# Kernel optimization log

Hardware: AMD Instinct MI355X
Metric: run time of the kernel (lower is better)

The kernel has to match this reference:

```python
import jax, jax.numpy as jnp
import numpy as np

Q = 0.25          # magnetic charge q
MAX_EIGEN = 2.0   # max_eigen default

N_NODES = 1024
N_EDGES = 32768
IN_DIM = 128


def setup_inputs() -> dict:
    key = jax.random.key(0)
    k1, k2, k3, k4 = jax.random.split(key, 4)
    features = jax.random.normal(k1, (N_NODES, IN_DIM), dtype=jnp.float32)
    edges = jax.random.randint(k2, (2, N_EDGES), 0, N_NODES, dtype=jnp.int64)
    w_e1 = jax.random.normal(k3, (1, IN_DIM), dtype=jnp.float32) * (1.0 / np.sqrt(IN_DIM))
    b_e1 = jax.random.normal(k4, (1,), dtype=jnp.float32) * 0.01
    return {"features": features, "edges": edges, "w_e1": w_e1, "b_e1": b_e1, "K": 4}


def reference(features, edges, w_e1, b_e1, K):
    N = features.shape[0]
    # e1: Linear(input_dim, 1), then squeeze -> per-node scalar potential p
    p = (features @ w_e1.T + b_e1)[:, 0]                       # [N]
    u, v = edges[0], edges[1]
    val = jnp.maximum(p[u] - p[v], 0.0)                        # [M]
    w = 1.0 + val
    directed = val > 0
    # val == 0 -> self loops (u,u),(v,v); val > 0 -> (u,v),(v,u); weight 1+val each
    rows = jnp.concatenate([u, v])
    cols = jnp.concatenate([jnp.where(directed, v, u), jnp.where(directed, u, v)])
    ww = jnp.concatenate([w, w])
    A = jnp.zeros((N, N), dtype=features.dtype).at[rows, cols].add(ww)
    A = A + jnp.eye(N, dtype=features.dtype)                   # unit-weight self loops (diag_eye)

    A_sym = 0.5 * (A + A.T)
    # symmetric degree normalization (norm=True)
    d = A_sym.sum(axis=0)
    d = jnp.where(d == 0, 1.0, d) ** -0.5
    A_sym = d[:, None] * A_sym * d[None, :]

    # magnetic phase: Theta = exp(2*pi*q*i*(A - A^T))
    Theta = jnp.exp((2j * jnp.pi * Q) * (A - A.T).astype(jnp.complex64))
    I = jnp.eye(N, dtype=jnp.complex64)
    L = I - Theta * A_sym.astype(jnp.complex64)                # D=I since norm=True
    L = (2.0 / MAX_EIGEN) * L - I                              # spectral rescale

    # Chebyshev recursion: T0 = I, T1 = L, T_k = 2 L T_{k-1} - T_{k-2}
    polys = [I, L]
    for _ in range(2, K + 1):
        polys.append(2.0 * (L @ polys[-1]) - polys[-2])
    L_real = jnp.stack([t.real for t in polys])                # [K+1, N, N]
    L_img = jnp.stack([t.imag for t in polys])                 # [K+1, N, N]
    return (L_real, L_img)
```

## Files before the change

kernel.cpp:

```cpp
#include <hip/hip_runtime.h>

#define NPTS 1024
#define NN (NPTS * NPTS)
#define NEDGE 32768
#define INDIM 128
#define PAD 72

typedef __attribute__((ext_vector_type(8))) short bf16x8;
typedef __attribute__((ext_vector_type(4))) float f32x4;

__device__ inline ushort f2bf(float x) {
    union { float f; unsigned u; } v; v.f = x;
    unsigned r = (v.u + 0x7FFF + ((v.u >> 16) & 1)) >> 16;
    return (ushort)r;
}

#define MFMA(a, b, c) __builtin_amdgcn_mfma_f32_16x16x32_bf16(a, b, c, 0, 0, 0)


__global__ void zeroA_p_kernel(float4* __restrict__ A4,
                               const float* __restrict__ feat,
                               const float* __restrict__ w,
                               const float* __restrict__ b,
                               float* __restrict__ p) {
    int t = threadIdx.x;
    A4[blockIdx.x * 256 + t] = make_float4(0.f, 0.f, 0.f, 0.f);
    if (blockIdx.x < 256) {
        int wid = t >> 6, lane = t & 63;
        int node = blockIdx.x * 4 + wid;
        const float* f = feat + node * INDIM;
        float s = f[lane] * w[lane] + f[lane + 64] * w[lane + 64];
#pragma unroll
        for (int off = 32; off; off >>= 1) s += __shfl_down(s, off);
        if (lane == 0) p[node] = s + b[0];
    }
}

__global__ void build_A_kernel(const int* __restrict__ eu, const int* __restrict__ ev,
                               const float* __restrict__ p, float* __restrict__ A) {
    int i = blockIdx.x * blockDim.x + threadIdx.x;
    if (i >= NEDGE) return;
    int u = eu[i], v = ev[i];
    float val = p[u] - p[v];
    if (val > 0.f) {
        float w = 1.f + val;
        atomicAdd(&A[u * NPTS + v], w);
        atomicAdd(&A[v * NPTS + u], w);
    } else {
        atomicAdd(&A[u * NPTS + u], 1.f);
        atomicAdd(&A[v * NPTS + v], 1.f);
    }
}

__global__ void row_deg_kernel(const float* __restrict__ A, float* __restrict__ dinv) {
    int wid = threadIdx.x >> 6, lane = threadIdx.x & 63;
    int row = blockIdx.x * 4 + wid;
    const float4* r4 = (const float4*)(A + (size_t)row * NPTS);
    float s = 0.f;
#pragma unroll
    for (int c = 0; c < 4; ++c) {
        float4 v = r4[c * 64 + lane];
        s += v.x + v.y + v.z + v.w;
    }
#pragma unroll
    for (int off = 32; off; off >>= 1) s += __shfl_down(s, off);
    if (lane == 0) dinv[row] = rsqrtf(s + 1.f);
}

__global__ void normalize_kernel(const float* __restrict__ A, const float* __restrict__ dinv,
                                 float* __restrict__ out, ushort* __restrict__ Mbf) {
    int idx4 = blockIdx.x * blockDim.x + threadIdx.x;
    int i = idx4 >> 8;
    int j = (idx4 & 255) * 4;
    size_t idx = (size_t)idx4 * 4;
    float di = dinv[i];
    float4 a = *(const float4*)(A + idx);
    float4 dj = *(const float4*)(dinv + j);
    float4 t0 = make_float4(0.f, 0.f, 0.f, 0.f);
    if (i == j) t0.x = 1.f;
    else if (i == j + 1) t0.y = 1.f;
    else if (i == j + 2) t0.z = 1.f;
    else if (i == j + 3) t0.w = 1.f;
    a.x += (i == j);
    a.y += (i == j + 1);
    a.z += (i == j + 2);
    a.w += (i == j + 3);
    float4 m;
    m.x = -(di * a.x * dj.x);
    m.y = -(di * a.y * dj.y);
    m.z = -(di * a.z * dj.z);
    m.w = -(di * a.w * dj.w);
    *(float4*)(out + idx) = t0;
    *(float4*)(out + NN + idx) = m;
    ushort mb[4] = {f2bf(m.x), f2bf(m.y), f2bf(m.z), f2bf(m.w)};
    *(uint2*)(Mbf + idx) = *(uint2*)mb;
}

__global__ __launch_bounds__(512) void gemm_S_kernel(const ushort* __restrict__ Mbf,
                                                     ushort* __restrict__ Sbf,
                                                     float* __restrict__ out) {
    __shared__ __align__(16) ushort smem[4 * 64 * PAD];
    ushort(*sA)[64][PAD] = (ushort(*)[64][PAD])smem;
    ushort(*sB)[64][PAD] = (ushort(*)[64][PAD])(smem + 2 * 64 * PAD);
    float* red = (float*)smem;

    int tid = threadIdx.x;
    int brow = blockIdx.y * 64, bcol = blockIdx.x * 64;
    int r = tid >> 3, j0 = (tid & 7) * 8;
    int wid = tid >> 6, lane = tid & 63;
    int h = wid >> 2, w4 = wid & 3;
    int wr = (w4 & 1) * 32, wc = (w4 >> 1) * 32;
    int fr = lane & 15, g = lane >> 4;

    const ushort* Arow = Mbf + (size_t)(brow + r) * NPTS;
    const ushort* Brow = Mbf + (size_t)(bcol + r) * NPTS;

    f32x4 acc[2][2] = {};
    float4 pa0 = *(const float4*)(Arow + j0);
    float4 pa1 = *(const float4*)(Arow + 64 + j0);
    float4 pb0 = *(const float4*)(Brow + j0);
    float4 pb1 = *(const float4*)(Brow + 64 + j0);

    for (int it = 0; it < 8; ++it) {
        __syncthreads();
        *(float4*)&sA[0][r][j0] = pa0;
        *(float4*)&sA[1][r][j0] = pa1;
        *(float4*)&sB[0][r][j0] = pb0;
        *(float4*)&sB[1][r][j0] = pb1;
        __syncthreads();
        if (it < 7) {
            int k0 = (it + 1) * 128;
            pa0 = *(const float4*)(Arow + k0 + j0);
            pa1 = *(const float4*)(Arow + k0 + 64 + j0);
            pb0 = *(const float4*)(Brow + k0 + j0);
            pb1 = *(const float4*)(Brow + k0 + 64 + j0);
        }
#pragma unroll
        for (int kc = 0; kc < 2; ++kc) {
            int kk = kc * 32 + g * 8;
            bf16x8 a0 = *(const bf16x8*)&sA[h][wr + fr][kk];
            bf16x8 a1 = *(const bf16x8*)&sA[h][wr + 16 + fr][kk];
            bf16x8 b0 = *(const bf16x8*)&sB[h][wc + fr][kk];
            bf16x8 b1 = *(const bf16x8*)&sB[h][wc + 16 + fr][kk];
            acc[0][0] = MFMA(a0, b0, acc[0][0]);
            acc[0][1] = MFMA(a0, b1, acc[0][1]);
            acc[1][0] = MFMA(a1, b0, acc[1][0]);
            acc[1][1] = MFMA(a1, b1, acc[1][1]);
        }
    }

    __syncthreads();
    if (h == 1) {
#pragma unroll
        for (int q = 0; q < 4; ++q)
            *(f32x4*)&red[q * 1024 + (w4 * 64 + lane) * 4] = acc[q >> 1][q & 1];
    }
    __syncthreads();
    if (h == 0) {
        float* T2 = out + (size_t)2 * NN;
#pragma unroll
        for (int mi = 0; mi < 2; ++mi) {
#pragma unroll
            for (int ni = 0; ni < 2; ++ni) {
                f32x4 o = *(f32x4*)&red[(mi * 2 + ni) * 1024 + (w4 * 64 + lane) * 4];
#pragma unroll
                for (int q = 0; q < 4; ++q) {
                    int row = brow + wr + mi * 16 + g * 4 + q;
                    int col = bcol + wc + ni * 16 + fr;
                    size_t idx = (size_t)row * NPTS + col;
                    float s = acc[mi][ni][q] + o[q];
                    T2[idx] = 2.f * s - (row == col ? 1.f : 0.f);
                    Sbf[idx] = f2bf(s);
                }
            }
        }
    }
}

__global__ __launch_bounds__(512) void gemm_T34_kernel(const ushort* __restrict__ Mbf,
                                                       const ushort* __restrict__ Sbf,
                                                       float* __restrict__ out,
                                                       int zimag) {
    if (zimag) {
        int bid = blockIdx.y * 16 + blockIdx.x;
        float4* z = (float4*)(out + (size_t)5 * NN) + (size_t)bid * 5120 + threadIdx.x;
#pragma unroll
        for (int i = 0; i < 10; ++i) z[i * 512] = make_float4(0.f, 0.f, 0.f, 0.f);
    }

    __shared__ __align__(16) ushort smem[6 * 64 * PAD];
    ushort(*sAS)[64][PAD] = (ushort(*)[64][PAD])smem;
    ushort(*sAM)[64][PAD] = (ushort(*)[64][PAD])(smem + 2 * 64 * PAD);
    ushort(*sB)[64][PAD] = (ushort(*)[64][PAD])(smem + 4 * 64 * PAD);
    float* red = (float*)smem;

    int tid = threadIdx.x;
    int brow = blockIdx.y * 64, bcol = blockIdx.x * 64;
    int r = tid >> 3, j0 = (tid & 7) * 8;
    int wid = tid >> 6, lane = tid & 63;
    int h = wid >> 2, w4 = wid & 3;
    int wr = (w4 & 1) * 32, wc = (w4 >> 1) * 32;
    int fr = lane & 15, g = lane >> 4;

    const ushort* ASrow = Sbf + (size_t)(brow + r) * NPTS;
    const ushort* AMrow = Mbf + (size_t)(brow + r) * NPTS;
    const ushort* Brow = Sbf + (size_t)(bcol + r) * NPTS;

    f32x4 accP[2][2] = {};
    f32x4 accR[2][2] = {};
    float4 ps0 = *(const float4*)(ASrow + j0);
    float4 ps1 = *(const float4*)(ASrow + 64 + j0);
    float4 pm0 = *(const float4*)(AMrow + j0);
    float4 pm1 = *(const float4*)(AMrow + 64 + j0);
    float4 pb0 = *(const float4*)(Brow + j0);
    float4 pb1 = *(const float4*)(Brow + 64 + j0);

    for (int it = 0; it < 8; ++it) {
        __syncthreads();
        *(float4*)&sAS[0][r][j0] = ps0;
        *(float4*)&sAS[1][r][j0] = ps1;
        *(float4*)&sAM[0][r][j0] = pm0;
        *(float4*)&sAM[1][r][j0] = pm1;
        *(float4*)&sB[0][r][j0] = pb0;
        *(float4*)&sB[1][r][j0] = pb1;
        __syncthreads();
        if (it < 7) {
            int k0 = (it + 1) * 128;
            ps0 = *(const float4*)(ASrow + k0 + j0);
            ps1 = *(const float4*)(ASrow + k0 + 64 + j0);
            pm0 = *(const float4*)(AMrow + k0 + j0);
            pm1 = *(const float4*)(AMrow + k0 + 64 + j0);
            pb0 = *(const float4*)(Brow + k0 + j0);
            pb1 = *(const float4*)(Brow + k0 + 64 + j0);
        }
#pragma unroll
        for (int kc = 0; kc < 2; ++kc) {
            int kk = kc * 32 + g * 8;
            bf16x8 b0 = *(const bf16x8*)&sB[h][wc + fr][kk];
            bf16x8 b1 = *(const bf16x8*)&sB[h][wc + 16 + fr][kk];
            bf16x8 s0 = *(const bf16x8*)&sAS[h][wr + fr][kk];
            bf16x8 s1 = *(const bf16x8*)&sAS[h][wr + 16 + fr][kk];
            accP[0][0] = MFMA(s0, b0, accP[0][0]);
            accP[0][1] = MFMA(s0, b1, accP[0][1]);
            accP[1][0] = MFMA(s1, b0, accP[1][0]);
            accP[1][1] = MFMA(s1, b1, accP[1][1]);
            bf16x8 m0 = *(const bf16x8*)&sAM[h][wr + fr][kk];
            bf16x8 m1 = *(const bf16x8*)&sAM[h][wr + 16 + fr][kk];
            accR[0][0] = MFMA(m0, b0, accR[0][0]);
            accR[0][1] = MFMA(m0, b1, accR[0][1]);
            accR[1][0] = MFMA(m1, b0, accR[1][0]);
            accR[1][1] = MFMA(m1, b1, accR[1][1]);
        }
    }

    __syncthreads();
    if (h == 1) {
#pragma unroll
        for (int q = 0; q < 4; ++q) {
            *(f32x4*)&red[q * 1024 + (w4 * 64 + lane) * 4] = accP[q >> 1][q & 1];
            *(f32x4*)&red[4096 + q * 1024 + (w4 * 64 + lane) * 4] = accR[q >> 1][q & 1];
        }
    }
    __syncthreads();
    if (h == 0) {
        float* T1 = out + (size_t)NN;
        float* T2 = out + (size_t)2 * NN;
        float* T3 = out + (size_t)3 * NN;
        float* T4 = out + (size_t)4 * NN;
#pragma unroll
        for (int mi = 0; mi < 2; ++mi) {
#pragma unroll
            for (int ni = 0; ni < 2; ++ni) {
                f32x4 oP = *(f32x4*)&red[(mi * 2 + ni) * 1024 + (w4 * 64 + lane) * 4];
                f32x4 oR = *(f32x4*)&red[4096 + (mi * 2 + ni) * 1024 + (w4 * 64 + lane) * 4];
#pragma unroll
                for (int q = 0; q < 4; ++q) {
                    int row = brow + wr + mi * 16 + g * 4 + q;
                    int col = bcol + wc + ni * 16 + fr;
                    size_t idx = (size_t)row * NPTS + col;
                    float sp = accP[mi][ni][q] + oP[q];
                    float sr = accR[mi][ni][q] + oR[q];
                    T4[idx] = 8.f * sp - 4.f * T2[idx] - (row == col ? 3.f : 0.f);
                    T3[idx] = 4.f * sr - 3.f * T1[idx];
                }
            }
        }
    }
}

__global__ void zero_kernel(float4* __restrict__ p, int n4) {
    int i = blockIdx.x * blockDim.x + threadIdx.x;
    if (i < n4) p[i] = make_float4(0.f, 0.f, 0.f, 0.f);
}


extern "C" void kernel_launch(void* const* d_in, const int* in_sizes, int n_in,
                              void* d_out, int out_size, void* d_ws, size_t ws_size,
                              hipStream_t stream) {
    const float* feat = (const float*)d_in[0];
    const int* edges = (const int*)d_in[1];
    const float* w_e1 = (const float*)d_in[2];
    const float* b_e1 = (const float*)d_in[3];
    float* out = (float*)d_out;

    const size_t need = (size_t)NN * 4 + (size_t)NN * 2 + (size_t)NN * 2 + NPTS * 8 + 256;
    float* A;
    ushort* Mbf;
    ushort* Sbf;
    float* p;
    float* dinv;
    int use_ws = (ws_size >= need);
    if (use_ws) {
        char* w = (char*)d_ws;
        A = (float*)w;        w += (size_t)NN * 4;
        Mbf = (ushort*)w;     w += (size_t)NN * 2;
        Sbf = (ushort*)w;     w += (size_t)NN * 2;
        p = (float*)w;        w += NPTS * 4;
        dinv = (float*)w;
    } else {
        A = out + (size_t)5 * NN;
        Mbf = (ushort*)(out + (size_t)6 * NN);
        Sbf = Mbf + NN;
        p = out + (size_t)7 * NN;
        dinv = p + NPTS;
    }

    zeroA_p_kernel<<<1024, 256, 0, stream>>>((float4*)A, feat, w_e1, b_e1, p);
    build_A_kernel<<<(NEDGE + 255) / 256, 256, 0, stream>>>(edges, edges + NEDGE, p, A);
    row_deg_kernel<<<256, 256, 0, stream>>>(A, dinv);
    normalize_kernel<<<NN / 4 / 256, 256, 0, stream>>>(A, dinv, out, Mbf);

    dim3 grid(16, 16);
    gemm_S_kernel<<<grid, 512, 0, stream>>>(Mbf, Sbf, out);
    gemm_T34_kernel<<<grid, 512, 0, stream>>>(Mbf, Sbf, out, use_ws);

    if (!use_ws) {
        zero_kernel<<<(5 * NN / 4 + 255) / 256, 256, 0, stream>>>(
            (float4*)(out + (size_t)5 * NN), 5 * NN / 4);
    }
}
```

Baseline: 48.49 us.

## Fuse whole pipeline into one cooperative kernel with grid syncs

Replaces the chain of separate launches (zero/projection, edge scatter, degree, normalize, two GEMMs) with a single cooperative mega-kernel of 256 blocks that separates the phases with grid.sync(). Node degrees are now accumulated with atomics during the edge scatter, which removes the row-degree reduction pass over A. The goal is to cut launch overhead and inter-kernel gaps. In exchange it adds grid-wide barrier cost, limits the GEMM phases to a fixed 256-block grid, and adds more atomic contention on the degree array. Degree accumulation now happens in a different order, so float sums may differ slightly.

```diff
diff --git a/kernel.cpp b/kernel.cpp
--- a/kernel.cpp
+++ b/kernel.cpp
@@ -1,4 +1,7 @@
 #include <hip/hip_runtime.h>
+#include <hip/hip_cooperative_groups.h>
+
+namespace cg = cooperative_groups;
 
 #define NPTS 1024
 #define NN (NPTS * NPTS)
@@ -16,6 +19,263 @@
 }
 
 #define MFMA(a, b, c) __builtin_amdgcn_mfma_f32_16x16x32_bf16(a, b, c, 0, 0, 0)
+
+__global__ __launch_bounds__(512) void mega_kernel(
+    const float* __restrict__ feat, const int* __restrict__ edges,
+    const float* __restrict__ w_e1, const float* __restrict__ b_e1,
+    float* __restrict__ out, float* __restrict__ A,
+    ushort* __restrict__ Mbf, ushort* __restrict__ Sbf,
+    float* __restrict__ p, float* __restrict__ dd, int zimag) {
+    cg::grid_group grid = cg::this_grid();
+    __shared__ __align__(16) ushort smem[6 * 64 * PAD];
+
+    int tid = threadIdx.x;
+    int bid = blockIdx.x;
+    int wid = tid >> 6, lane = tid & 63;
+
+    {
+        float4* A4 = (float4*)A;
+#pragma unroll
+        for (int i = 0; i < 2; ++i)
+            A4[bid * 1024 + i * 512 + tid] = make_float4(0.f, 0.f, 0.f, 0.f);
+        if (bid == 0 && tid < 256) ((float4*)dd)[tid] = make_float4(0.f, 0.f, 0.f, 0.f);
+        if (wid < 4) {
+            int node = bid * 4 + wid;
+            const float* f = feat + node * INDIM;
+            float s = f[lane] * w_e1[lane] + f[lane + 64] * w_e1[lane + 64];
+#pragma unroll
+            for (int off = 32; off; off >>= 1) s += __shfl_down(s, off);
+            if (lane == 0) p[node] = s + b_e1[0];
+        }
+    }
+    grid.sync();
+
+    if (tid < 128) {
+        int i = bid * 128 + tid;
+        int u = edges[i], v = edges[NEDGE + i];
+        float val = p[u] - p[v];
+        if (val > 0.f) {
+            float w = 1.f + val;
+            atomicAdd(&A[u * NPTS + v], w);
+            atomicAdd(&A[v * NPTS + u], w);
+            atomicAdd(&dd[u], w);
+            atomicAdd(&dd[v], w);
+        } else {
+            atomicAdd(&A[u * NPTS + u], 1.f);
+            atomicAdd(&A[v * NPTS + v], 1.f);
+            atomicAdd(&dd[u], 1.f);
+            atomicAdd(&dd[v], 1.f);
+        }
+    }
+    grid.sync();
+
+    {
+#pragma unroll
+        for (int it = 0; it < 2; ++it) {
+            int idx4 = bid * 1024 + it * 512 + tid;
+            int i = idx4 >> 8;
+            int j = (idx4 & 255) * 4;
+            size_t idx = (size_t)idx4 * 4;
+            float di = rsqrtf(dd[i] + 1.f);
+            float4 a = *(const float4*)(A + idx);
+            float4 d4 = *(const float4*)(dd + j);
+            float4 t0 = make_float4(0.f, 0.f, 0.f, 0.f);
+            if (i == j) t0.x = 1.f;
+            else if (i == j + 1) t0.y = 1.f;
+            else if (i == j + 2) t0.z = 1.f;
+            else if (i == j + 3) t0.w = 1.f;
+            a.x += (i == j);
+            a.y += (i == j + 1);
+            a.z += (i == j + 2);
+            a.w += (i == j + 3);
+            float4 m;
+            m.x = -(di * a.x * rsqrtf(d4.x + 1.f));
+            m.y = -(di * a.y * rsqrtf(d4.y + 1.f));
+            m.z = -(di * a.z * rsqrtf(d4.z + 1.f));
+            m.w = -(di * a.w * rsqrtf(d4.w + 1.f));
+            *(float4*)(out + idx) = t0;
+            *(float4*)(out + NN + idx) = m;
+            ushort mb[4] = {f2bf(m.x), f2bf(m.y), f2bf(m.z), f2bf(m.w)};
+            *(uint2*)(Mbf + idx) = *(uint2*)mb;
+        }
+    }
+    grid.sync();
+
+    int brow = (bid >> 4) * 64, bcol = (bid & 15) * 64;
+    int r = tid >> 3, j0 = (tid & 7) * 8;
+    int h = wid >> 2, w4 = wid & 3;
+    int wr = (w4 & 1) * 32, wc = (w4 >> 1) * 32;
+    int fr = lane & 15, g = lane >> 4;
+
+    {
+        ushort(*sA)[64][PAD] = (ushort(*)[64][PAD])smem;
+        ushort(*sB)[64][PAD] = (ushort(*)[64][PAD])(smem + 2 * 64 * PAD);
+        float* red = (float*)smem;
+
+        const ushort* Arow = Mbf + (size_t)(brow + r) * NPTS;
+        const ushort* Brow = Mbf + (size_t)(bcol + r) * NPTS;
+
+        f32x4 acc[2][2] = {};
+        float4 pa0 = *(const float4*)(Arow + j0);
+        float4 pa1 = *(const float4*)(Arow + 64 + j0);
+        float4 pb0 = *(const float4*)(Brow + j0);
+        float4 pb1 = *(const float4*)(Brow + 64 + j0);
+
+        for (int it = 0; it < 8; ++it) {
+            __syncthreads();
+            *(float4*)&sA[0][r][j0] = pa0;
+            *(float4*)&sA[1][r][j0] = pa1;
+            *(float4*)&sB[0][r][j0] = pb0;
+            *(float4*)&sB[1][r][j0] = pb1;
+            __syncthreads();
+            if (it < 7) {
+                int k0 = (it + 1) * 128;
+                pa0 = *(const float4*)(Arow + k0 + j0);
+                pa1 = *(const float4*)(Arow + k0 + 64 + j0);
+                pb0 = *(const float4*)(Brow + k0 + j0);
+                pb1 = *(const float4*)(Brow + k0 + 64 + j0);
+            }
+#pragma unroll
+            for (int kc = 0; kc < 2; ++kc) {
+                int kk = kc * 32 + g * 8;
+                bf16x8 a0 = *(const bf16x8*)&sA[h][wr + fr][kk];
+                bf16x8 a1 = *(const bf16x8*)&sA[h][wr + 16 + fr][kk];
+                bf16x8 b0 = *(const bf16x8*)&sB[h][wc + fr][kk];
+                bf16x8 b1 = *(const bf16x8*)&sB[h][wc + 16 + fr][kk];
+                acc[0][0] = MFMA(a0, b0, acc[0][0]);
+                acc[0][1] = MFMA(a0, b1, acc[0][1]);
+                acc[1][0] = MFMA(a1, b0, acc[1][0]);
+                acc[1][1] = MFMA(a1, b1, acc[1][1]);
+            }
+        }
+
+        __syncthreads();
+        if (h == 1) {
+#pragma unroll
+            for (int q = 0; q < 4; ++q)
+                *(f32x4*)&red[q * 1024 + (w4 * 64 + lane) * 4] = acc[q >> 1][q & 1];
+        }
+        __syncthreads();
+        if (h == 0) {
+            float* T2 = out + (size_t)2 * NN;
+#pragma unroll
+            for (int mi = 0; mi < 2; ++mi) {
+#pragma unroll
+                for (int ni = 0; ni < 2; ++ni) {
+                    f32x4 o = *(f32x4*)&red[(mi * 2 + ni) * 1024 + (w4 * 64 + lane) * 4];
+#pragma unroll
+                    for (int q = 0; q < 4; ++q) {
+                        int row = brow + wr + mi * 16 + g * 4 + q;
+                        int col = bcol + wc + ni * 16 + fr;
+                        size_t idx = (size_t)row * NPTS + col;
+                        float s = acc[mi][ni][q] + o[q];
+                        T2[idx] = 2.f * s - (row == col ? 1.f : 0.f);
+                        Sbf[idx] = f2bf(s);
+                    }
+                }
+            }
+        }
+    }
+    grid.sync();
+
+    {
+        if (zimag) {
+            float4* z = (float4*)(out + (size_t)5 * NN) + (size_t)bid * 5120 + tid;
+#pragma unroll
+            for (int i = 0; i < 10; ++i) z[i * 512] = make_float4(0.f, 0.f, 0.f, 0.f);
+        }
+
+        ushort(*sAS)[64][PAD] = (ushort(*)[64][PAD])smem;
+        ushort(*sAM)[64][PAD] = (ushort(*)[64][PAD])(smem + 2 * 64 * PAD);
+        ushort(*sB)[64][PAD] = (ushort(*)[64][PAD])(smem + 4 * 64 * PAD);
+        float* red = (float*)smem;
+
+        const ushort* ASrow = Sbf + (size_t)(brow + r) * NPTS;
+        const ushort* AMrow = Mbf + (size_t)(brow + r) * NPTS;
+        const ushort* Brow = Sbf + (size_t)(bcol + r) * NPTS;
+
+        f32x4 accP[2][2] = {};
+        f32x4 accR[2][2] = {};
+        float4 ps0 = *(const float4*)(ASrow + j0);
+        float4 ps1 = *(const float4*)(ASrow + 64 + j0);
+        float4 pm0 = *(const float4*)(AMrow + j0);
+        float4 pm1 = *(const float4*)(AMrow + 64 + j0);
+        float4 pb0 = *(const float4*)(Brow + j0);
+        float4 pb1 = *(const float4*)(Brow + 64 + j0);
+
+        for (int it = 0; it < 8; ++it) {
+            __syncthreads();
+            *(float4*)&sAS[0][r][j0] = ps0;
+            *(float4*)&sAS[1][r][j0] = ps1;
+            *(float4*)&sAM[0][r][j0] = pm0;
+            *(float4*)&sAM[1][r][j0] = pm1;
+            *(float4*)&sB[0][r][j0] = pb0;
+            *(float4*)&sB[1][r][j0] = pb1;
+            __syncthreads();
+            if (it < 7) {
+                int k0 = (it + 1) * 128;
+                ps0 = *(const float4*)(ASrow + k0 + j0);
+                ps1 = *(const float4*)(ASrow + k0 + 64 + j0);
+                pm0 = *(const float4*)(AMrow + k0 + j0);
+                pm1 = *(const float4*)(AMrow + k0 + 64 + j0);
+                pb0 = *(const float4*)(Brow + k0 + j0);
+                pb1 = *(const float4*)(Brow + k0 + 64 + j0);
+            }
+#pragma unroll
+            for (int kc = 0; kc < 2; ++kc) {
+                int kk = kc * 32 + g * 8;
+                bf16x8 b0 = *(const bf16x8*)&sB[h][wc + fr][kk];
+                bf16x8 b1 = *(const bf16x8*)&sB[h][wc + 16 + fr][kk];
+                bf16x8 s0 = *(const bf16x8*)&sAS[h][wr + fr][kk];
+                bf16x8 s1 = *(const bf16x8*)&sAS[h][wr + 16 + fr][kk];
+                accP[0][0] = MFMA(s0, b0, accP[0][0]);
+                accP[0][1] = MFMA(s0, b1, accP[0][1]);
+                accP[1][0] = MFMA(s1, b0, accP[1][0]);
+                accP[1][1] = MFMA(s1, b1, accP[1][1]);
+                bf16x8 m0 = *(const bf16x8*)&sAM[h][wr + fr][kk];
+                bf16x8 m1 = *(const bf16x8*)&sAM[h][wr + 16 + fr][kk];
+                accR[0][0] = MFMA(m0, b0, accR[0][0]);
+                accR[0][1] = MFMA(m0, b1, accR[0][1]);
+                accR[1][0] = MFMA(m1, b0, accR[1][0]);
+                accR[1][1] = MFMA(m1, b1, accR[1][1]);
+            }
+        }
+
+        __syncthreads();
+        if (h == 1) {
+#pragma unroll
+            for (int q = 0; q < 4; ++q) {
+                *(f32x4*)&red[q * 1024 + (w4 * 64 + lane) * 4] = accP[q >> 1][q & 1];
+                *(f32x4*)&red[4096 + q * 1024 + (w4 * 64 + lane) * 4] = accR[q >> 1][q & 1];
+            }
+        }
+        __syncthreads();
+        if (h == 0) {
+            float* T1 = out + (size_t)NN;
+            float* T2 = out + (size_t)2 * NN;
+            float* T3 = out + (size_t)3 * NN;
+            float* T4 = out + (size_t)4 * NN;
+#pragma unroll
+            for (int mi = 0; mi < 2; ++mi) {
+#pragma unroll
+                for (int ni = 0; ni < 2; ++ni) {
+                    f32x4 oP = *(f32x4*)&red[(mi * 2 + ni) * 1024 + (w4 * 64 + lane) * 4];
+                    f32x4 oR = *(f32x4*)&red[4096 + (mi * 2 + ni) * 1024 + (w4 * 64 + lane) * 4];
+#pragma unroll
+                    for (int q = 0; q < 4; ++q) {
+                        int row = brow + wr + mi * 16 + g * 4 + q;
+                        int col = bcol + wc + ni * 16 + fr;
+                        size_t idx = (size_t)row * NPTS + col;
+                        float sp = accP[mi][ni][q] + oP[q];
+                        float sr = accR[mi][ni][q] + oR[q];
+                        T4[idx] = 8.f * sp - 4.f * T2[idx] - (row == col ? 3.f : 0.f);
+                        T3[idx] = 4.f * sr - 3.f * T1[idx];
+                    }
+                }
+            }
+        }
+    }
+}
 
 
 __global__ void zeroA_p_kernel(float4* __restrict__ A4,
@@ -37,7 +297,8 @@
 }
 
 __global__ void build_A_kernel(const int* __restrict__ eu, const int* __restrict__ ev,
-                               const float* __restrict__ p, float* __restrict__ A) {
+                               const float* __restrict__ p, float* __restrict__ A,
+                               float* __restrict__ dd) {
     int i = blockIdx.x * blockDim.x + threadIdx.x;
     if (i >= NEDGE) return;
     int u = eu[i], v = ev[i];
@@ -46,36 +307,29 @@
         float w = 1.f + val;
         atomicAdd(&A[u * NPTS + v], w);
         atomicAdd(&A[v * NPTS + u], w);
+        atomicAdd(&dd[u], w);
+        atomicAdd(&dd[v], w);
     } else {
         atomicAdd(&A[u * NPTS + u], 1.f);
         atomicAdd(&A[v * NPTS + v], 1.f);
-    }
-}
-
-__global__ void row_deg_kernel(const float* __restrict__ A, float* __restrict__ dinv) {
-    int wid = threadIdx.x >> 6, lane = threadIdx.x & 63;
-    int row = blockIdx.x * 4 + wid;
-    const float4* r4 = (const float4*)(A + (size_t)row * NPTS);
-    float s = 0.f;
-#pragma unroll
-    for (int c = 0; c < 4; ++c) {
-        float4 v = r4[c * 64 + lane];
-        s += v.x + v.y + v.z + v.w;
-    }
-#pragma unroll
-    for (int off = 32; off; off >>= 1) s += __shfl_down(s, off);
-    if (lane == 0) dinv[row] = rsqrtf(s + 1.f);
-}
-
-__global__ void normalize_kernel(const float* __restrict__ A, const float* __restrict__ dinv,
+        atomicAdd(&dd[u], 1.f);
+        atomicAdd(&dd[v], 1.f);
+    }
+}
+
+__global__ void zero_d_kernel(float4* __restrict__ d4) {
+    if (blockIdx.x == 0 && threadIdx.x < 256) d4[threadIdx.x] = make_float4(0.f, 0.f, 0.f, 0.f);
+}
+
+__global__ void normalize_kernel(const float* __restrict__ A, const float* __restrict__ dd,
                                  float* __restrict__ out, ushort* __restrict__ Mbf) {
     int idx4 = blockIdx.x * blockDim.x + threadIdx.x;
     int i = idx4 >> 8;
     int j = (idx4 & 255) * 4;
     size_t idx = (size_t)idx4 * 4;
-    float di = dinv[i];
+    float di = rsqrtf(dd[i] + 1.f);
     float4 a = *(const float4*)(A + idx);
-    float4 dj = *(const float4*)(dinv + j);
+    float4 d4 = *(const float4*)(dd + j);
     float4 t0 = make_float4(0.f, 0.f, 0.f, 0.f);
     if (i == j) t0.x = 1.f;
     else if (i == j + 1) t0.y = 1.f;
@@ -86,10 +340,10 @@
     a.z += (i == j + 2);
     a.w += (i == j + 3);
     float4 m;
-    m.x = -(di * a.x * dj.x);
-    m.y = -(di * a.y * dj.y);
-    m.z = -(di * a.z * dj.z);
-    m.w = -(di * a.w * dj.w);
+    m.x = -(di * a.x * rsqrtf(d4.x + 1.f));
+    m.y = -(di * a.y * rsqrtf(d4.y + 1.f));
+    m.z = -(di * a.z * rsqrtf(d4.z + 1.f));
+    m.w = -(di * a.w * rsqrtf(d4.w + 1.f));
     *(float4*)(out + idx) = t0;
     *(float4*)(out + NN + idx) = m;
     ushort mb[4] = {f2bf(m.x), f2bf(m.y), f2bf(m.z), f2bf(m.w)};
@@ -308,7 +562,7 @@
     ushort* Mbf;
     ushort* Sbf;
     float* p;
-    float* dinv;
+    float* dd;
     int use_ws = (ws_size >= need);
     if (use_ws) {
         char* w = (char*)d_ws;
@@ -316,19 +570,32 @@
         Mbf = (ushort*)w;     w += (size_t)NN * 2;
         Sbf = (ushort*)w;     w += (size_t)NN * 2;
         p = (float*)w;        w += NPTS * 4;
-        dinv = (float*)w;
+        dd = (float*)w;
     } else {
         A = out + (size_t)5 * NN;
         Mbf = (ushort*)(out + (size_t)6 * NN);
         Sbf = Mbf + NN;
         p = out + (size_t)7 * NN;
-        dinv = p + NPTS;
+        dd = p + NPTS;
+    }
+
+    void* kargs[] = {(void*)&feat, (void*)&edges, (void*)&w_e1, (void*)&b_e1,
+                     (void*)&out, (void*)&A, (void*)&Mbf, (void*)&Sbf,
+                     (void*)&p, (void*)&dd, (void*)&use_ws};
+    hipError_t err = hipLaunchCooperativeKernel((void*)mega_kernel, dim3(256), dim3(512),
+                                                kargs, 0, stream);
+    if (err == hipSuccess) {
+        if (!use_ws) {
+            zero_kernel<<<(5 * NN / 4 + 255) / 256, 256, 0, stream>>>(
+                (float4*)(out + (size_t)5 * NN), 5 * NN / 4);
+        }
+        return;
     }
 
     zeroA_p_kernel<<<1024, 256, 0, stream>>>((float4*)A, feat, w_e1, b_e1, p);
-    build_A_kernel<<<(NEDGE + 255) / 256, 256, 0, stream>>>(edges, edges + NEDGE, p, A);
-    row_deg_kernel<<<256, 256, 0, stream>>>(A, dinv);
-    normalize_kernel<<<NN / 4 / 256, 256, 0, stream>>>(A, dinv, out, Mbf);
+    zero_d_kernel<<<1, 256, 0, stream>>>((float4*)dd);
+    build_A_kernel<<<(NEDGE + 255) / 256, 256, 0, stream>>>(edges, edges + NEDGE, p, A, dd);
+    normalize_kernel<<<NN / 4 / 256, 256, 0, stream>>>(A, dd, out, Mbf);
 
     dim3 grid(16, 16);
     gemm_S_kernel<<<grid, 512, 0, stream>>>(Mbf, Sbf, out);
```

Result: slower. 167.4 us (+245.3%).
